# Optimization experiments

Measured on AMD Instinct MI355X. Metric: run time of the kernel, lower is better.

Reference implementation:

```python
import jax, jax.numpy as jnp
import numpy as np

BSZ, H, P, L = 8, 512, 128, 8192
DT_MIN, DT_MAX = 1e-3, 1e-1


def setup_inputs() -> dict:
    key = jax.random.key(0)
    ks = jax.random.split(key, 6)
    inp = {}
    inp["input_sequence"] = jax.random.normal(ks[0], (BSZ, 1, H, 1, L), jnp.float32)
    # HiPPO-like init: negative real parts, pi*k imaginary parts
    inp["Lambda_re"] = -jax.random.uniform(ks[1], (P,), jnp.float32, 0.1, 1.0)
    inp["Lambda_im"] = jnp.pi * jnp.arange(P, dtype=jnp.float32)
    # lecun_normal-ish: fan_in = H for B, fan_in = P for C (real+imag parts)
    inp["B"] = jax.random.normal(ks[2], (P, H, 2), jnp.float32) / np.float32(np.sqrt(2 * H))
    inp["C"] = jax.random.normal(ks[3], (H, P, 2), jnp.float32) / np.float32(np.sqrt(2 * P))
    inp["D"] = jax.random.normal(ks[4], (H,), jnp.float32)
    u01 = jax.random.uniform(ks[5], (P, 1), jnp.float32)
    inp["log_step"] = u01 * np.float32(np.log(DT_MAX) - np.log(DT_MIN)) + np.float32(np.log(DT_MIN))
    return inp


def _binary_operator(q_i, q_j):
    A_i, b_i = q_i
    A_j, b_j = q_j
    return (A_j * A_i, A_j * b_i + b_j)


def reference(input_sequence, Lambda_re, Lambda_im, B, C, D, log_step):
    # (bsz, 1, H, 1, L) -> (bsz, L, H)
    u = input_sequence[:, 0, :, 0].transpose(0, 2, 1)

    Lambda = Lambda_re + 1j * Lambda_im                      # (P,)
    B_tilde = B[..., 0] + 1j * B[..., 1]                     # (P, H)
    C_tilde = C[..., 0] + 1j * C[..., 1]                     # (H, P)
    step = jnp.exp(log_step[:, 0])                           # (P,)

    # zero-order hold discretization
    Lambda_bar = jnp.exp(Lambda * step)                      # (P,)
    B_bar = ((Lambda_bar - 1.0) / Lambda)[:, None] * B_tilde # (P, H)

    Bu = jnp.einsum('blh,ph->blp', u, B_bar)                 # (bsz, L, P) complex
    Lambda_elems = jnp.broadcast_to(Lambda_bar, Bu.shape)
    _, xs = jax.lax.associative_scan(_binary_operator, (Lambda_elems, Bu), axis=1)

    # conj_sym=True -> factor of 2 on the real part of emissions
    ys = 2.0 * jnp.einsum('blp,hp->blh', xs, C_tilde).real + D * u
    ys = jax.nn.gelu(ys, approximate=False)

    # back to (bsz, 1, H, 1, L)
    return ys.transpose(0, 2, 1)[:, None, :, None, :]
```

## Files before the change

### kernel.cpp

```cpp
#include <hip/hip_runtime.h>
#include <hip/hip_bf16.h>
#include <cmath>

namespace {
constexpr int Pn = 128;
constexpr int Hn = 512;
constexpr int Ln = 8192;
constexpr int BS = 8;
constexpr size_t OFF_BMAT = 2048;
constexpr size_t OFF_CMAT = 264192;
constexpr size_t OFF_END  = 526336;
constexpr size_t OFF_CAR  = 2623488;
constexpr size_t HEADB    = 4720640;
constexpr size_t SZ_BU = (size_t)256 * Ln * 4;
}

typedef __attribute__((ext_vector_type(4))) float f32x4;
typedef __attribute__((ext_vector_type(8))) short bf16x8;

static __device__ inline short f2bf(float x) {
  __hip_bfloat16 h = __float2bfloat16(x);
  return *(short*)&h;
}

static __device__ inline void async_copy16(const void* g, void* l) {
  __builtin_amdgcn_global_load_lds(
      (const __attribute__((address_space(1))) unsigned int*)g,
      (__attribute__((address_space(3))) unsigned int*)l, 16, 0, 0);
}

__global__ void precompute_kernel(const float* __restrict__ Lre,
                                  const float* __restrict__ Lim,
                                  const float* __restrict__ Bin,
                                  const float* __restrict__ Cin,
                                  const float* __restrict__ lstep,
                                  float* __restrict__ Lam,
                                  __hip_bfloat16* __restrict__ Bmat,
                                  __hip_bfloat16* __restrict__ Cmat) {
  int tid = blockIdx.x * blockDim.x + threadIdx.x;
  if (tid < 2 * Pn * Hn) {
    int r = tid >> 9;
    int h = tid & (Hn - 1);
    int p = r & (Pn - 1);
    float st = expf(lstep[p]);
    float lr = Lre[p], li = Lim[p];
    float er = expf(lr * st);
    float cr = er * cosf(li * st);
    float ci = er * sinf(li * st);
    float nr = cr - 1.0f, ni = ci;
    float inv = 1.0f / (lr * lr + li * li);
    float wr = (nr * lr + ni * li) * inv;
    float wi = (ni * lr - nr * li) * inv;
    float btr = Bin[(p * Hn + h) * 2 + 0];
    float bti = Bin[(p * Hn + h) * 2 + 1];
    float val = (r < Pn) ? (wr * btr - wi * bti) : (wr * bti + wi * btr);
    Bmat[tid] = __float2bfloat16(val);
  } else if (tid < 4 * Pn * Hn) {
    int j = tid - 2 * Pn * Hn;
    int h = j >> 8;
    int c = j & 255;
    int p = c & (Pn - 1);
    float v = (c < Pn) ? 2.0f * Cin[(h * Pn + p) * 2 + 0]
                       : -2.0f * Cin[(h * Pn + p) * 2 + 1];
    Cmat[j] = __float2bfloat16(v);
  } else if (tid < 4 * Pn * Hn + 512) {
    int j = tid - 4 * Pn * Hn;
    int p = j & 127;
    int sel = j >> 7;
    float st = expf(lstep[p]);
    float lr = Lre[p], li = Lim[p];
    float sc = (sel < 2) ? st : 32.0f * st;
    float er = expf(lr * sc);
    Lam[(sel >> 1) * 256 + (sel & 1) * 128 + p] =
        (sel & 1) ? er * sinf(li * sc) : er * cosf(li * sc);
  }
}

__global__ __launch_bounds__(256) void gemm1_kernel(
    const __hip_bfloat16* __restrict__ Amat,
    const float* __restrict__ U,
    float* __restrict__ Bu,
    int b0) {
  __shared__ __align__(16) short As[128 * 32];
  __shared__ __align__(16) short Bs[128 * 40];
  const int t = threadIdx.x;
  const int lane = t & 63, w = t >> 6;
  const int wm = w >> 1, wn = w & 1;
  const int n0 = blockIdx.x * 128;
  const int m0 = blockIdx.y * 128;
  const int bz = blockIdx.z;
  const float* Ub = U + (size_t)(b0 + bz) * Hn * Ln;

  const int srow = lane >> 2, scol = (lane & 3) * 16;
  const int bn = t & 127, bkg = t >> 7;

  f32x4 acc[4][4] = {};
  for (int k0 = 0; k0 < Hn; k0 += 32) {
#pragma unroll
    for (int I2 = 0; I2 < 2; I2++) {
      int I = 2 * w + I2;
      async_copy16((const char*)(Amat + (size_t)(m0 + 16 * I + srow) * Hn + k0) + scol,
                   (char*)As + I * 1024);
    }
#pragma unroll
    for (int p = 0; p < 2; p++) {
      int kb = p * 16 + bkg * 8;
      float v[8];
#pragma unroll
      for (int j = 0; j < 8; j++)
        v[j] = Ub[(size_t)(k0 + kb + j) * Ln + n0 + bn];
      bf16x8 pk;
#pragma unroll
      for (int j = 0; j < 8; j++) pk[j] = f2bf(v[j]);
      *(bf16x8*)&Bs[bn * 40 + kb] = pk;
    }
    __syncthreads();
    bf16x8 af[4], bfr[4];
#pragma unroll
    for (int mt = 0; mt < 4; mt++)
      af[mt] = *(const bf16x8*)&As[(64 * wm + 16 * mt + (lane & 15)) * 32 + (lane >> 4) * 8];
#pragma unroll
    for (int nt = 0; nt < 4; nt++)
      bfr[nt] = *(const bf16x8*)&Bs[(64 * wn + 16 * nt + (lane & 15)) * 40 + (lane >> 4) * 8];
#pragma unroll
    for (int mt = 0; mt < 4; mt++)
#pragma unroll
      for (int nt = 0; nt < 4; nt++)
        acc[mt][nt] = __builtin_amdgcn_mfma_f32_16x16x32_bf16(
            af[mt], bfr[nt], acc[mt][nt], 0, 0, 0);
    __syncthreads();
  }
  const int row4 = (lane >> 4) * 4, col = lane & 15;
  float* Bub = Bu + (size_t)bz * Ln * 256;
#pragma unroll
  for (int mt = 0; mt < 4; mt++)
#pragma unroll
    for (int nt = 0; nt < 4; nt++) {
      int n = n0 + 64 * wn + 16 * nt + col;
      int m = m0 + 64 * wm + 16 * mt + row4;
      *(f32x4*)&Bub[(size_t)n * 256 + m] = acc[mt][nt];
    }
}

__global__ __launch_bounds__(256) void scan_ends_kernel(const float* __restrict__ Bu,
                                                        const float* __restrict__ Lam,
                                                        float* __restrict__ End) {
  const int bz = blockIdx.y;
  const int t = threadIdx.x;
  const int c = blockIdx.x * 2 + (t >> 7);
  const int p = t & 127;
  const float Ar = Lam[p], Ai = Lam[128 + p];
  const float* base = Bu + ((size_t)bz * Ln + (size_t)c * 32) * 256;
  float br[32], bi[32];
#pragma unroll
  for (int i = 0; i < 32; i++) br[i] = base[(size_t)i * 256 + p];
#pragma unroll
  for (int i = 0; i < 32; i++) bi[i] = base[(size_t)i * 256 + 128 + p];
  float xr = 0.f, xi = 0.f;
#pragma unroll
  for (int i = 0; i < 32; i++) {
    float nr = fmaf(Ar, xr, fmaf(-Ai, xi, br[i]));
    float ni = fmaf(Ar, xi, fmaf(Ai, xr, bi[i]));
    xr = nr; xi = ni;
  }
  float* E = End + ((size_t)bz * 256 + c) * 256;
  E[p] = xr;
  E[128 + p] = xi;
}

__global__ __launch_bounds__(128) void carry_kernel(const float* __restrict__ End,
                                                    float* __restrict__ Carry,
                                                    const float* __restrict__ Lam) {
  const int bz = blockIdx.x;
  const int p = threadIdx.x;
  const float a32r = Lam[256 + p], a32i = Lam[384 + p];
  const float* E = End + (size_t)bz * 256 * 256;
  float* C = Carry + (size_t)bz * 256 * 256;
  float xr = 0.f, xi = 0.f;
  float er0[4], ei0[4], er1[4], ei1[4];
#pragma unroll
  for (int q = 0; q < 4; q++) {
    er0[q] = E[(size_t)q * 256 + p];
    ei0[q] = E[(size_t)q * 256 + 128 + p];
  }
  for (int c0 = 0; c0 < 256; c0 += 8) {
#pragma unroll
    for (int q = 0; q < 4; q++) {
      er1[q] = E[(size_t)(c0 + 4 + q) * 256 + p];
      ei1[q] = E[(size_t)(c0 + 4 + q) * 256 + 128 + p];
    }
#pragma unroll
    for (int q = 0; q < 4; q++) {
      C[(size_t)(c0 + q) * 256 + p] = xr;
      C[(size_t)(c0 + q) * 256 + 128 + p] = xi;
      float nr = fmaf(a32r, xr, fmaf(-a32i, xi, er0[q]));
      float ni = fmaf(a32r, xi, fmaf(a32i, xr, ei0[q]));
      xr = nr; xi = ni;
    }
#pragma unroll
    for (int q = 0; q < 4; q++) {
      int cn = c0 + 8 + q;
      if (cn < 256) {
        er0[q] = E[(size_t)cn * 256 + p];
        ei0[q] = E[(size_t)cn * 256 + 128 + p];
      }
    }
#pragma unroll
    for (int q = 0; q < 4; q++) {
      C[(size_t)(c0 + 4 + q) * 256 + p] = xr;
      C[(size_t)(c0 + 4 + q) * 256 + 128 + p] = xi;
      float nr = fmaf(a32r, xr, fmaf(-a32i, xi, er1[q]));
      float ni = fmaf(a32r, xi, fmaf(a32i, xr, ei1[q]));
      xr = nr; xi = ni;
    }
  }
}

__global__ __launch_bounds__(256) void scan_apply_kernel(float* __restrict__ Bu,
                                                         const float* __restrict__ Lam,
                                                         const float* __restrict__ Carry) {
  const int bz = blockIdx.y;
  const int t = threadIdx.x;
  const int c = blockIdx.x * 2 + (t >> 7);
  const int p = t & 127;
  const float Ar = Lam[p], Ai = Lam[128 + p];
  float* base = Bu + ((size_t)bz * Ln + (size_t)c * 32) * 256;
  const float* Cg = Carry + ((size_t)bz * 256 + c) * 256;
  float br[32], bi[32];
#pragma unroll
  for (int i = 0; i < 32; i++) br[i] = base[(size_t)i * 256 + p];
#pragma unroll
  for (int i = 0; i < 32; i++) bi[i] = base[(size_t)i * 256 + 128 + p];
  float xr = Cg[p], xi = Cg[128 + p];
#pragma unroll
  for (int i = 0; i < 32; i++) {
    float nr = fmaf(Ar, xr, fmaf(-Ai, xi, br[i]));
    float ni = fmaf(Ar, xi, fmaf(Ai, xr, bi[i]));
    xr = nr; xi = ni;
    base[(size_t)i * 256 + p] = nr;
    base[(size_t)i * 256 + 128 + p] = ni;
  }
}

__global__ __launch_bounds__(256) void gemm2_kernel(
    const __hip_bfloat16* __restrict__ Cmat,
    const float* __restrict__ Xs,
    const float* __restrict__ U,
    const float* __restrict__ Dv,
    float* __restrict__ Out, int b0) {
  __shared__ __align__(16) short As[128 * 32];
  __shared__ __align__(16) short Bs[128 * 40];
  const int t = threadIdx.x;
  const int lane = t & 63, w = t >> 6;
  const int wm = w >> 1, wn = w & 1;
  const int n0 = blockIdx.x * 128;
  const int m0 = blockIdx.y * 128;
  const int bz = blockIdx.z;
  const int b = b0 + bz;

  const int srow = lane >> 2, scol = (lane & 3) * 16;
  const int bn = t & 127, bkg = t >> 7;
  const float* Xrow = Xs + ((size_t)bz * Ln + n0 + bn) * 256;

  f32x4 acc[4][4] = {};
  for (int k0 = 0; k0 < 256; k0 += 32) {
#pragma unroll
    for (int I2 = 0; I2 < 2; I2++) {
      int I = 2 * w + I2;
      async_copy16((const char*)(Cmat + (size_t)(m0 + 16 * I + srow) * 256 + k0) + scol,
                   (char*)As + I * 1024);
    }
#pragma unroll
    for (int p2 = 0; p2 < 2; p2++) {
      int kb = p2 * 16 + bkg * 8;
      f32x4 x0 = *(const f32x4*)&Xrow[k0 + kb];
      f32x4 x1 = *(const f32x4*)&Xrow[k0 + kb + 4];
      bf16x8 pk;
#pragma unroll
      for (int q = 0; q < 4; q++) { pk[q] = f2bf(x0[q]); pk[4 + q] = f2bf(x1[q]); }
      *(bf16x8*)&Bs[bn * 40 + kb] = pk;
    }
    __syncthreads();
    bf16x8 af[4], bfr[4];
#pragma unroll
    for (int mt = 0; mt < 4; mt++)
      af[mt] = *(const bf16x8*)&As[(64 * wm + 16 * mt + (lane & 15)) * 32 + (lane >> 4) * 8];
#pragma unroll
    for (int nt = 0; nt < 4; nt++)
      bfr[nt] = *(const bf16x8*)&Bs[(64 * wn + 16 * nt + (lane & 15)) * 40 + (lane >> 4) * 8];
#pragma unroll
    for (int mt = 0; mt < 4; mt++)
#pragma unroll
      for (int nt = 0; nt < 4; nt++)
        acc[mt][nt] = __builtin_amdgcn_mfma_f32_16x16x32_bf16(
            af[mt], bfr[nt], acc[mt][nt], 0, 0, 0);
    __syncthreads();
  }
  const int row4 = (lane >> 4) * 4, col = lane & 15;
#pragma unroll
  for (int mt = 0; mt < 4; mt++) {
#pragma unroll
    for (int r = 0; r < 4; r++) {
      int h = m0 + 64 * wm + 16 * mt + row4 + r;
      float dh = Dv[h];
      const float* Urow = U + ((size_t)b * Hn + h) * Ln;
      float* Orow = Out + ((size_t)b * Hn + h) * Ln;
#pragma unroll
      for (int nt = 0; nt < 4; nt++) {
        int n = n0 + 64 * wn + 16 * nt + col;
        float y = acc[mt][nt][r] + dh * Urow[n];
        float u2 = y * (0.7978845608f + 0.0356774081f * y * y);
        Orow[n] = y / (1.0f + __expf(-2.0f * u2));
      }
    }
  }
}

extern "C" void kernel_launch(void* const* d_in, const int* in_sizes, int n_in,
                              void* d_out, int out_size, void* d_ws, size_t ws_size,
                              hipStream_t stream) {
  const float* U   = (const float*)d_in[0];
  const float* Lre = (const float*)d_in[1];
  const float* Lim = (const float*)d_in[2];
  const float* Bin = (const float*)d_in[3];
  const float* Cin = (const float*)d_in[4];
  const float* Dv  = (const float*)d_in[5];
  const float* ls  = (const float*)d_in[6];
  float* out = (float*)d_out;

  char* wsb = (char*)d_ws;
  float* Lam = (float*)wsb;
  __hip_bfloat16* Bmat = (__hip_bfloat16*)(wsb + OFF_BMAT);
  __hip_bfloat16* Cmat = (__hip_bfloat16*)(wsb + OFF_CMAT);
  float* End = (float*)(wsb + OFF_END);
  float* Cy  = (float*)(wsb + OFF_CAR);
  float* Bu  = (float*)(wsb + HEADB);

  int NB = 8;
  while (NB > 1 && ws_size < HEADB + (size_t)NB * SZ_BU)
    NB >>= 1;

  precompute_kernel<<<(4 * Pn * Hn + 512 + 255) / 256, 256, 0, stream>>>(
      Lre, Lim, Bin, Cin, ls, Lam, Bmat, Cmat);

  for (int b0 = 0; b0 < BS; b0 += NB) {
    gemm1_kernel<<<dim3(Ln / 128, 2, NB), 256, 0, stream>>>(Bmat, U, Bu, b0);
    scan_ends_kernel<<<dim3(128, NB), 256, 0, stream>>>(Bu, Lam, End);
    carry_kernel<<<dim3(NB), 128, 0, stream>>>(End, Cy, Lam);
    scan_apply_kernel<<<dim3(128, NB), 256, 0, stream>>>(Bu, Lam, Cy);
    gemm2_kernel<<<dim3(Ln / 128, Hn / 128, NB), 256, 0, stream>>>(
        Cmat, Bu, U, Dv, out, b0);
  }
}
```

Baseline: 376.8 us.

## Retile gemm1 to cover all 256 outputs per block and coalesce gemm2 loads

gemm1 now gives each block all 256 M rows (the full complex P dimension) over a 64-column N tile. Each input U element is therefore loaded and converted to bf16 once instead of twice across the two M blocks, at the cost of a larger A tile in shared memory. gemm2's staging of Xs is rearranged so that four consecutive threads read contiguous 16-byte chunks of the same row, which gives more coalesced global reads. The gemm2 layout writes bf16x4 halves into LDS, which may cause more bank conflicts.

```diff
diff --git a/kernel.cpp b/kernel.cpp
--- a/kernel.cpp
+++ b/kernel.cpp
@@ -17,6 +17,7 @@
 
 typedef __attribute__((ext_vector_type(4))) float f32x4;
 typedef __attribute__((ext_vector_type(8))) short bf16x8;
+typedef __attribute__((ext_vector_type(4))) short bf16x4;
 
 static __device__ inline short f2bf(float x) {
   __hip_bfloat16 h = __float2bfloat16(x);
@@ -81,47 +82,43 @@
     const float* __restrict__ U,
     float* __restrict__ Bu,
     int b0) {
-  __shared__ __align__(16) short As[128 * 32];
-  __shared__ __align__(16) short Bs[128 * 40];
+  __shared__ __align__(16) short As[256 * 32];
+  __shared__ __align__(16) short Bs[64 * 40];
   const int t = threadIdx.x;
   const int lane = t & 63, w = t >> 6;
-  const int wm = w >> 1, wn = w & 1;
-  const int n0 = blockIdx.x * 128;
-  const int m0 = blockIdx.y * 128;
+  const int n0 = blockIdx.x * 64;
   const int bz = blockIdx.z;
   const float* Ub = U + (size_t)(b0 + bz) * Hn * Ln;
 
   const int srow = lane >> 2, scol = (lane & 3) * 16;
-  const int bn = t & 127, bkg = t >> 7;
+  const int bn = t & 63, bkg = t >> 6;
 
   f32x4 acc[4][4] = {};
   for (int k0 = 0; k0 < Hn; k0 += 32) {
 #pragma unroll
-    for (int I2 = 0; I2 < 2; I2++) {
-      int I = 2 * w + I2;
-      async_copy16((const char*)(Amat + (size_t)(m0 + 16 * I + srow) * Hn + k0) + scol,
+    for (int I2 = 0; I2 < 4; I2++) {
+      int I = 4 * w + I2;
+      async_copy16((const char*)(Amat + (size_t)(16 * I + srow) * Hn + k0) + scol,
                    (char*)As + I * 1024);
     }
-#pragma unroll
-    for (int p = 0; p < 2; p++) {
-      int kb = p * 16 + bkg * 8;
+    {
       float v[8];
 #pragma unroll
       for (int j = 0; j < 8; j++)
-        v[j] = Ub[(size_t)(k0 + kb + j) * Ln + n0 + bn];
+        v[j] = Ub[(size_t)(k0 + bkg * 8 + j) * Ln + n0 + bn];
       bf16x8 pk;
 #pragma unroll
       for (int j = 0; j < 8; j++) pk[j] = f2bf(v[j]);
-      *(bf16x8*)&Bs[bn * 40 + kb] = pk;
+      *(bf16x8*)&Bs[bn * 40 + bkg * 8] = pk;
     }
     __syncthreads();
     bf16x8 af[4], bfr[4];
 #pragma unroll
     for (int mt = 0; mt < 4; mt++)
-      af[mt] = *(const bf16x8*)&As[(64 * wm + 16 * mt + (lane & 15)) * 32 + (lane >> 4) * 8];
+      af[mt] = *(const bf16x8*)&As[(64 * w + 16 * mt + (lane & 15)) * 32 + (lane >> 4) * 8];
 #pragma unroll
     for (int nt = 0; nt < 4; nt++)
-      bfr[nt] = *(const bf16x8*)&Bs[(64 * wn + 16 * nt + (lane & 15)) * 40 + (lane >> 4) * 8];
+      bfr[nt] = *(const bf16x8*)&Bs[(16 * nt + (lane & 15)) * 40 + (lane >> 4) * 8];
 #pragma unroll
     for (int mt = 0; mt < 4; mt++)
 #pragma unroll
@@ -136,8 +133,8 @@
   for (int mt = 0; mt < 4; mt++)
 #pragma unroll
     for (int nt = 0; nt < 4; nt++) {
-      int n = n0 + 64 * wn + 16 * nt + col;
-      int m = m0 + 64 * wm + 16 * mt + row4;
+      int n = n0 + 16 * nt + col;
+      int m = 64 * w + 16 * mt + row4;
       *(f32x4*)&Bub[(size_t)n * 256 + m] = acc[mt][nt];
     }
 }
@@ -259,8 +256,9 @@
   const int b = b0 + bz;
 
   const int srow = lane >> 2, scol = (lane & 3) * 16;
-  const int bn = t & 127, bkg = t >> 7;
-  const float* Xrow = Xs + ((size_t)bz * Ln + n0 + bn) * 256;
+  const int krow = t >> 2;
+  const int kq = t & 3;
+  const float* Xbase = Xs + ((size_t)bz * Ln + n0) * 256;
 
   f32x4 acc[4][4] = {};
   for (int k0 = 0; k0 < 256; k0 += 32) {
@@ -271,14 +269,16 @@
                    (char*)As + I * 1024);
     }
 #pragma unroll
-    for (int p2 = 0; p2 < 2; p2++) {
-      int kb = p2 * 16 + bkg * 8;
-      f32x4 x0 = *(const f32x4*)&Xrow[k0 + kb];
-      f32x4 x1 = *(const f32x4*)&Xrow[k0 + kb + 4];
-      bf16x8 pk;
-#pragma unroll
-      for (int q = 0; q < 4; q++) { pk[q] = f2bf(x0[q]); pk[4 + q] = f2bf(x1[q]); }
-      *(bf16x8*)&Bs[bn * 40 + kb] = pk;
+    for (int ro = 0; ro < 2; ro++) {
+      int row = ro * 64 + krow;
+      const float* src = Xbase + (size_t)row * 256 + k0 + kq * 4;
+      f32x4 x0 = *(const f32x4*)src;
+      f32x4 x1 = *(const f32x4*)(src + 16);
+      bf16x4 a, c;
+#pragma unroll
+      for (int q = 0; q < 4; q++) { a[q] = f2bf(x0[q]); c[q] = f2bf(x1[q]); }
+      *(bf16x4*)&Bs[row * 40 + kq * 4] = a;
+      *(bf16x4*)&Bs[row * 40 + 16 + kq * 4] = c;
     }
     __syncthreads();
     bf16x8 af[4], bfr[4];
@@ -344,7 +344,7 @@
       Lre, Lim, Bin, Cin, ls, Lam, Bmat, Cmat);
 
   for (int b0 = 0; b0 < BS; b0 += NB) {
-    gemm1_kernel<<<dim3(Ln / 128, 2, NB), 256, 0, stream>>>(Bmat, U, Bu, b0);
+    gemm1_kernel<<<dim3(Ln / 64, 1, NB), 256, 0, stream>>>(Bmat, U, Bu, b0);
     scan_ends_kernel<<<dim3(128, NB), 256, 0, stream>>>(Bu, Lam, End);
     carry_kernel<<<dim3(NB), 128, 0, stream>>>(End, Cy, Lam);
     scan_apply_kernel<<<dim3(128, NB), 256, 0, stream>>>(Bu, Lam, Cy);
```

Result: no change. 373.2 us (-1.0%).
